# Performance work log

Hardware: AMD Instinct MI355X
Metric: run time of the kernel (lower is better)

## Reference

```python
import jax, jax.numpy as jnp
import numpy as np

B, S, N, U, E, L = 32, 32, 128, 64, 2, 2
N_STEPS = 3
NUM_CLASSES = 5


def setup_inputs() -> dict:
    key = jax.random.key(0)
    ks = jax.random.split(key, 10)
    input_seq = jax.random.normal(ks[0], (B, S, N * U), dtype=jnp.float32)
    seq_lengths = jax.random.randint(ks[1], (B,), 0, S)
    # per-edge-type adjacency, scaled ~row-stochastic for numerical sanity
    adjacency_matrix = jax.random.uniform(ks[2], (B, E, N, N), dtype=jnp.float32) / N
    sc = 1.0 / np.sqrt(U)
    W_msg = jax.random.normal(ks[3], (L, E, U, U), dtype=jnp.float32) * sc
    b_msg = jnp.zeros((L, U), dtype=jnp.float32)
    Wg = jax.random.normal(ks[4], (L, 3, U, U), dtype=jnp.float32) * sc  # gates from aggregated messages
    Ug = jax.random.normal(ks[5], (L, 3, U, U), dtype=jnp.float32) * sc  # gates from hidden state
    bg = jnp.zeros((L, 3, U), dtype=jnp.float32)
    fc_w = jax.random.normal(ks[6], (U, NUM_CLASSES), dtype=jnp.float32) * sc
    fc_b = jnp.zeros((NUM_CLASSES,), dtype=jnp.float32)
    return {
        "input_seq": input_seq, "seq_lengths": seq_lengths,
        "adjacency_matrix": adjacency_matrix,
        "W_msg": W_msg, "b_msg": b_msg, "Wg": Wg, "Ug": Ug, "bg": bg,
        "fc_w": fc_w, "fc_b": fc_b,
    }


def _ggnn_layer(h, A, W_msg_l, b_msg_l, Wg_l, Ug_l, bg_l):
    # h: [S,B,N,U], A: [B,E,N,N] (shared across timesteps)
    for _ in range(N_STEPS):
        # typed message passing: sum_e A_e @ h @ W_e
        a = jnp.einsum('benm,sbmu,euv->sbnv', A, h, W_msg_l) + b_msg_l
        g_a = jnp.einsum('sbnu,guv->gsbnv', a, Wg_l)  # [3,S,B,N,U]
        z = jax.nn.sigmoid(g_a[0] + h @ Ug_l[0] + bg_l[0])
        r = jax.nn.sigmoid(g_a[1] + h @ Ug_l[1] + bg_l[1])
        c = jnp.tanh(g_a[2] + (r * h) @ Ug_l[2] + bg_l[2])
        h = (1.0 - z) * h + z * c
    return h


def reference(input_seq, seq_lengths, adjacency_matrix, W_msg, b_msg, Wg, Ug, bg, fc_w, fc_b):
    # encoder: hidden state is NOT carried across timesteps in the original
    # (cell is called with current input only), so timesteps are vectorized.
    cur = input_seq.reshape(B, S, N, U).transpose(1, 0, 2, 3)  # [S,B,N,U]
    for l in range(L):
        cur = _ggnn_layer(cur, adjacency_matrix, W_msg[l], b_msg[l], Wg[l], Ug[l], bg[l])
    out = cur.transpose(1, 0, 2, 3)  # [B,S,N,U]
    idx = jnp.clip(seq_lengths - 1, 0, S - 1)
    last = out[jnp.arange(B), idx]  # [B,N,U] (last relevant timestep)
    # dropout is identity in eval mode
    logits = jax.nn.relu(last) @ fc_w + fc_b  # [B,N,C]
    return jnp.max(logits, axis=1)  # [B,C]
```

## Files before the change

kernel.cpp:

```cpp
#include <hip/hip_runtime.h>

#define B 32
#define S 32
#define N 128
#define U 64
#define E 2
#define NCLS 5


__device__ __forceinline__ float sigmoid_f(float x) {
    return __fdividef(1.f, 1.f + __expf(-x));
}
__device__ __forceinline__ float tanh_f(float x) {
    float t = __expf(-2.f * fabsf(x));
    float y = __fdividef(1.f - t, 1.f + t);
    return copysignf(y, x);
}
__device__ __forceinline__ float bcast(float v, int u) {
    return __uint_as_float(__builtin_amdgcn_readlane(__float_as_uint(v), u));
}

template <int FIRST, int LAST>
__global__ __launch_bounds__(256, 4) void k_step(
    const float* __restrict__ x, const int* __restrict__ lens,
    const float* __restrict__ hin, float* __restrict__ hout,
    const float* __restrict__ A, const float* __restrict__ Wmsg,
    const float* __restrict__ bmsg, const float* __restrict__ Wg,
    const float* __restrict__ Ug, const float* __restrict__ bg,
    const float* __restrict__ fcw, float* __restrict__ partial, int l) {
    __shared__ float red[4 * NCLS];
    int tid = threadIdx.x;
    int wave = tid >> 6, lane = tid & 63;
    int b = blockIdx.x >> 5;
    int j = blockIdx.x & 31;
    int row = __builtin_amdgcn_readfirstlane(j * 4 + wave);

    const float* __restrict__ hsrc;
    if (FIRST) {
        int idx = lens[b] - 1;
        idx = idx < 0 ? 0 : (idx > S - 1 ? S - 1 : idx);
        hsrc = x + (size_t)(b * S + idx) * N * U;
    } else {
        hsrc = hin + (size_t)b * N * U;
    }

    float hv = hsrc[row * U + lane];

    float s0 = 0.f, s1 = 0.f;
    {
        const float4* A0 = (const float4*)(A + (((size_t)b * E + 0) * N + row) * N);
        const float4* A1 = (const float4*)(A + (((size_t)b * E + 1) * N + row) * N);
#pragma unroll 8
        for (int m4 = 0; m4 < N / 4; ++m4) {
            float4 a0 = A0[m4], a1 = A1[m4];
            float q0 = hsrc[(m4 * 4 + 0) * U + lane];
            float q1 = hsrc[(m4 * 4 + 1) * U + lane];
            float q2 = hsrc[(m4 * 4 + 2) * U + lane];
            float q3 = hsrc[(m4 * 4 + 3) * U + lane];
            s0 = fmaf(a0.x, q0, s0); s0 = fmaf(a0.y, q1, s0);
            s0 = fmaf(a0.z, q2, s0); s0 = fmaf(a0.w, q3, s0);
            s1 = fmaf(a1.x, q0, s1); s1 = fmaf(a1.y, q1, s1);
            s1 = fmaf(a1.z, q2, s1); s1 = fmaf(a1.w, q3, s1);
        }
    }

    float av = bmsg[l * U + lane];
    {
        const float* W0 = Wmsg + (size_t)(l * E + 0) * U * U + lane;
        const float* W1 = W0 + U * U;
#pragma unroll 16
        for (int u = 0; u < U; ++u) {
            av = fmaf(bcast(s0, u), W0[u * U], av);
        }
#pragma unroll 16
        for (int u = 0; u < U; ++u) {
            av = fmaf(bcast(s1, u), W1[u * U], av);
        }
    }

    const float* Wg0 = Wg + (size_t)l * 3 * U * U + lane;
    const float* Wg1 = Wg0 + U * U;
    const float* Wg2 = Wg1 + U * U;
    const float* Ug0 = Ug + (size_t)l * 3 * U * U + lane;
    const float* Ug1 = Ug0 + U * U;
    const float* Ug2 = Ug1 + U * U;
    float accz = bg[(l * 3 + 0) * U + lane];
    float accr = bg[(l * 3 + 1) * U + lane];
    float accc = bg[(l * 3 + 2) * U + lane];
#pragma unroll 16
    for (int u = 0; u < U; ++u) {
        float w0 = Wg0[u * U], w1 = Wg1[u * U], w2 = Wg2[u * U];
        float g0 = Ug0[u * U], g1 = Ug1[u * U];
        float a = bcast(av, u);
        float h = bcast(hv, u);
        accz = fmaf(a, w0, accz); accz = fmaf(h, g0, accz);
        accr = fmaf(a, w1, accr); accr = fmaf(h, g1, accr);
        accc = fmaf(a, w2, accc);
    }
    float rg = sigmoid_f(accr);
    float rh = rg * hv;
#pragma unroll 16
    for (int u = 0; u < U; ++u) {
        accc = fmaf(bcast(rh, u), Ug2[u * U], accc);
    }
    float zg = sigmoid_f(accz);
    float hn = (1.f - zg) * hv + zg * tanh_f(accc);

    if (!LAST) {
        hout[((size_t)b * N + row) * U + lane] = hn;
    } else {
        float lg[NCLS];
        float rv = hn > 0.f ? hn : 0.f;
#pragma unroll
        for (int c = 0; c < NCLS; c++) {
            lg[c] = rv * fcw[lane * NCLS + c];
        }
#pragma unroll
        for (int off = 32; off; off >>= 1) {
#pragma unroll
            for (int c = 0; c < NCLS; c++) {
                lg[c] += __shfl_xor(lg[c], off, 64);
            }
        }
        if (lane == 0) {
#pragma unroll
            for (int c = 0; c < NCLS; c++) red[wave * NCLS + c] = lg[c];
        }
        __syncthreads();
        if (tid < NCLS) {
            float m = red[tid];
            for (int w = 1; w < 4; ++w) m = fmaxf(m, red[w * NCLS + tid]);
            partial[(size_t)(b * 32 + j) * NCLS + tid] = m;
        }
    }
}

__global__ void k_final(const float* __restrict__ partial, const float* __restrict__ fcb,
                        float* __restrict__ out) {
    int b = blockIdx.x, c = threadIdx.x;
    if (c < NCLS) {
        float m = -3.4e38f;
        for (int jj = 0; jj < 32; ++jj)
            m = fmaxf(m, partial[(size_t)(b * 32 + jj) * NCLS + c]);
        out[b * NCLS + c] = m + fcb[c];
    }
}

extern "C" void kernel_launch(void* const* d_in, const int* in_sizes, int n_in,
                              void* d_out, int out_size, void* d_ws, size_t ws_size,
                              hipStream_t stream) {
    const float* x    = (const float*)d_in[0];
    const int*   lens = (const int*)d_in[1];
    const float* A    = (const float*)d_in[2];
    const float* Wmsg = (const float*)d_in[3];
    const float* bmsg = (const float*)d_in[4];
    const float* Wg   = (const float*)d_in[5];
    const float* Ug   = (const float*)d_in[6];
    const float* bg   = (const float*)d_in[7];
    const float* fcw  = (const float*)d_in[8];
    const float* fcb  = (const float*)d_in[9];
    float* out = (float*)d_out;

    float* hA      = (float*)d_ws;
    float* hB      = hA + (size_t)B * N * U;
    float* partial = hB + (size_t)B * N * U;

    k_step<1, 0><<<B * 32, 256, 0, stream>>>(x, lens, nullptr, hA, A, Wmsg, bmsg, Wg, Ug, bg, fcw, partial, 0);
    k_step<0, 0><<<B * 32, 256, 0, stream>>>(x, lens, hA, hB, A, Wmsg, bmsg, Wg, Ug, bg, fcw, partial, 0);
    k_step<0, 0><<<B * 32, 256, 0, stream>>>(x, lens, hB, hA, A, Wmsg, bmsg, Wg, Ug, bg, fcw, partial, 0);
    k_step<0, 0><<<B * 32, 256, 0, stream>>>(x, lens, hA, hB, A, Wmsg, bmsg, Wg, Ug, bg, fcw, partial, 1);
    k_step<0, 0><<<B * 32, 256, 0, stream>>>(x, lens, hB, hA, A, Wmsg, bmsg, Wg, Ug, bg, fcw, partial, 1);
    k_step<0, 1><<<B * 32, 256, 0, stream>>>(x, lens, hA, hB, A, Wmsg, bmsg, Wg, Ug, bg, fcw, partial, 1);
    k_final<<<B, 64, 0, stream>>>(partial, fcb, out);
}
```

Before: 226.4 us.

## Fuse all GGNN steps into one persistent kernel with per-batch flag barriers

Replaces six step launches plus a final reduction with a single persistent kernel of 128 blocks (4 per batch). Each wave now handles 4 rows so weight loads are reused across rows. Blocks of the same batch synchronize between steps through an atomic counter in workspace, reset by a memset before launch. This removes launch gaps and the final kernel, but cuts the grid to 128 blocks, lowering parallelism, and relies on all four blocks of a batch being resident at once. The spin loop gives up after a fixed iteration count.

```diff
diff --git a/kernel.cpp b/kernel.cpp
--- a/kernel.cpp
+++ b/kernel.cpp
@@ -6,6 +6,8 @@
 #define U 64
 #define E 2
 #define NCLS 5
+#define NBLK 4
+#define RPW 4
 
 
 __device__ __forceinline__ float sigmoid_f(float x) {
@@ -20,129 +22,180 @@
     return __uint_as_float(__builtin_amdgcn_readlane(__float_as_uint(v), u));
 }
 
-template <int FIRST, int LAST>
-__global__ __launch_bounds__(256, 4) void k_step(
+__global__ __launch_bounds__(512) void k_all(
     const float* __restrict__ x, const int* __restrict__ lens,
-    const float* __restrict__ hin, float* __restrict__ hout,
+    float* __restrict__ hA, float* __restrict__ hB,
     const float* __restrict__ A, const float* __restrict__ Wmsg,
     const float* __restrict__ bmsg, const float* __restrict__ Wg,
     const float* __restrict__ Ug, const float* __restrict__ bg,
-    const float* __restrict__ fcw, float* __restrict__ partial, int l) {
-    __shared__ float red[4 * NCLS];
+    const float* __restrict__ fcw, const float* __restrict__ fcb,
+    float* __restrict__ partial, unsigned int* __restrict__ flags,
+    float* __restrict__ out) {
+    __shared__ float red[8 * NCLS];
     int tid = threadIdx.x;
     int wave = tid >> 6, lane = tid & 63;
-    int b = blockIdx.x >> 5;
-    int j = blockIdx.x & 31;
-    int row = __builtin_amdgcn_readfirstlane(j * 4 + wave);
-
-    const float* __restrict__ hsrc;
-    if (FIRST) {
-        int idx = lens[b] - 1;
-        idx = idx < 0 ? 0 : (idx > S - 1 ? S - 1 : idx);
-        hsrc = x + (size_t)(b * S + idx) * N * U;
-    } else {
-        hsrc = hin + (size_t)b * N * U;
-    }
-
-    float hv = hsrc[row * U + lane];
-
-    float s0 = 0.f, s1 = 0.f;
-    {
-        const float4* A0 = (const float4*)(A + (((size_t)b * E + 0) * N + row) * N);
-        const float4* A1 = (const float4*)(A + (((size_t)b * E + 1) * N + row) * N);
+    int b = blockIdx.x >> 2;
+    int q = blockIdx.x & 3;
+    int n0 = __builtin_amdgcn_readfirstlane(q * 32 + wave * RPW);
+
+    int idx = lens[b] - 1;
+    idx = idx < 0 ? 0 : (idx > S - 1 ? S - 1 : idx);
+    const float* xsrc = x + (size_t)(b * S + idx) * N * U;
+    float* h0 = hA + (size_t)b * N * U;
+    float* h1 = hB + (size_t)b * N * U;
+    unsigned int* flg = flags + b * 32;
+
+    for (int step = 0; step < 6; ++step) {
+        int l = step >= 3 ? 1 : 0;
+        const float* hsrc = (step == 0) ? xsrc : ((step & 1) ? h0 : h1);
+        float* hdst = (step & 1) ? h1 : h0;
+
+        float hv[RPW];
+#pragma unroll
+        for (int r = 0; r < RPW; ++r) hv[r] = hsrc[(n0 + r) * U + lane];
+
+        float s[RPW][E];
+#pragma unroll
+        for (int r = 0; r < RPW; ++r) { s[r][0] = 0.f; s[r][1] = 0.f; }
+        {
+            const float4* Ap[E][RPW];
+#pragma unroll
+            for (int e = 0; e < E; ++e)
+#pragma unroll
+                for (int r = 0; r < RPW; ++r)
+                    Ap[e][r] = (const float4*)(A + (((size_t)b * E + e) * N + n0 + r) * N);
+#pragma unroll 2
+            for (int m4 = 0; m4 < N / 4; ++m4) {
+                float q0 = hsrc[(m4 * 4 + 0) * U + lane];
+                float q1 = hsrc[(m4 * 4 + 1) * U + lane];
+                float q2 = hsrc[(m4 * 4 + 2) * U + lane];
+                float q3 = hsrc[(m4 * 4 + 3) * U + lane];
+#pragma unroll
+                for (int e = 0; e < E; ++e)
+#pragma unroll
+                    for (int r = 0; r < RPW; ++r) {
+                        float4 a = Ap[e][r][m4];
+                        s[r][e] = fmaf(a.x, q0, s[r][e]);
+                        s[r][e] = fmaf(a.y, q1, s[r][e]);
+                        s[r][e] = fmaf(a.z, q2, s[r][e]);
+                        s[r][e] = fmaf(a.w, q3, s[r][e]);
+                    }
+            }
+        }
+
+        float bm = bmsg[l * U + lane];
+        float av[RPW];
+#pragma unroll
+        for (int r = 0; r < RPW; ++r) av[r] = bm;
+        {
+            const float* W0 = Wmsg + (size_t)(l * E + 0) * U * U + lane;
+            const float* W1 = W0 + U * U;
+#pragma unroll 16
+            for (int u = 0; u < U; ++u) {
+                float w = W0[u * U];
+#pragma unroll
+                for (int r = 0; r < RPW; ++r) av[r] = fmaf(bcast(s[r][0], u), w, av[r]);
+            }
+#pragma unroll 16
+            for (int u = 0; u < U; ++u) {
+                float w = W1[u * U];
+#pragma unroll
+                for (int r = 0; r < RPW; ++r) av[r] = fmaf(bcast(s[r][1], u), w, av[r]);
+            }
+        }
+
+        const float* Wg0 = Wg + (size_t)l * 3 * U * U + lane;
+        const float* Wg1 = Wg0 + U * U;
+        const float* Wg2 = Wg1 + U * U;
+        const float* Ug0 = Ug + (size_t)l * 3 * U * U + lane;
+        const float* Ug1 = Ug0 + U * U;
+        const float* Ug2 = Ug1 + U * U;
+        float bz = bg[(l * 3 + 0) * U + lane];
+        float br = bg[(l * 3 + 1) * U + lane];
+        float bcc = bg[(l * 3 + 2) * U + lane];
+        float accz[RPW], accr[RPW], accc[RPW];
+#pragma unroll
+        for (int r = 0; r < RPW; ++r) { accz[r] = bz; accr[r] = br; accc[r] = bcc; }
 #pragma unroll 8
-        for (int m4 = 0; m4 < N / 4; ++m4) {
-            float4 a0 = A0[m4], a1 = A1[m4];
-            float q0 = hsrc[(m4 * 4 + 0) * U + lane];
-            float q1 = hsrc[(m4 * 4 + 1) * U + lane];
-            float q2 = hsrc[(m4 * 4 + 2) * U + lane];
-            float q3 = hsrc[(m4 * 4 + 3) * U + lane];
-            s0 = fmaf(a0.x, q0, s0); s0 = fmaf(a0.y, q1, s0);
-            s0 = fmaf(a0.z, q2, s0); s0 = fmaf(a0.w, q3, s0);
-            s1 = fmaf(a1.x, q0, s1); s1 = fmaf(a1.y, q1, s1);
-            s1 = fmaf(a1.z, q2, s1); s1 = fmaf(a1.w, q3, s1);
-        }
-    }
-
-    float av = bmsg[l * U + lane];
-    {
-        const float* W0 = Wmsg + (size_t)(l * E + 0) * U * U + lane;
-        const float* W1 = W0 + U * U;
+        for (int u = 0; u < U; ++u) {
+            float w0 = Wg0[u * U], w1 = Wg1[u * U], w2 = Wg2[u * U];
+            float g0 = Ug0[u * U], g1 = Ug1[u * U];
+#pragma unroll
+            for (int r = 0; r < RPW; ++r) {
+                float a = bcast(av[r], u);
+                float h = bcast(hv[r], u);
+                accz[r] = fmaf(a, w0, accz[r]); accz[r] = fmaf(h, g0, accz[r]);
+                accr[r] = fmaf(a, w1, accr[r]); accr[r] = fmaf(h, g1, accr[r]);
+                accc[r] = fmaf(a, w2, accc[r]);
+            }
+        }
+        float rh[RPW];
+#pragma unroll
+        for (int r = 0; r < RPW; ++r) rh[r] = sigmoid_f(accr[r]) * hv[r];
 #pragma unroll 16
         for (int u = 0; u < U; ++u) {
-            av = fmaf(bcast(s0, u), W0[u * U], av);
-        }
-#pragma unroll 16
-        for (int u = 0; u < U; ++u) {
-            av = fmaf(bcast(s1, u), W1[u * U], av);
-        }
+            float g2 = Ug2[u * U];
+#pragma unroll
+            for (int r = 0; r < RPW; ++r) accc[r] = fmaf(bcast(rh[r], u), g2, accc[r]);
+        }
+        float hn[RPW];
+#pragma unroll
+        for (int r = 0; r < RPW; ++r) {
+            float zg = sigmoid_f(accz[r]);
+            hn[r] = (1.f - zg) * hv[r] + zg * tanh_f(accc[r]);
+        }
+
+        if (step < 5) {
+#pragma unroll
+            for (int r = 0; r < RPW; ++r) hdst[(n0 + r) * U + lane] = hn[r];
+        } else {
+            float lg[RPW][NCLS];
+#pragma unroll
+            for (int r = 0; r < RPW; ++r) {
+                float rv = hn[r] > 0.f ? hn[r] : 0.f;
+#pragma unroll
+                for (int c = 0; c < NCLS; ++c) lg[r][c] = rv * fcw[lane * NCLS + c];
+            }
+#pragma unroll
+            for (int off = 32; off; off >>= 1)
+#pragma unroll
+                for (int r = 0; r < RPW; ++r)
+#pragma unroll
+                    for (int c = 0; c < NCLS; ++c) lg[r][c] += __shfl_xor(lg[r][c], off, 64);
+            if (lane == 0) {
+#pragma unroll
+                for (int c = 0; c < NCLS; ++c)
+                    red[wave * NCLS + c] =
+                        fmaxf(fmaxf(lg[0][c], lg[1][c]), fmaxf(lg[2][c], lg[3][c]));
+            }
+            __syncthreads();
+            if (tid < NCLS) {
+                float m = red[tid];
+                for (int w = 1; w < 8; ++w) m = fmaxf(m, red[w * NCLS + tid]);
+                partial[(size_t)(b * NBLK + q) * NCLS + tid] = m;
+            }
+        }
+
+        __syncthreads();
+        if (tid == 0) {
+            __threadfence();
+            atomicAdd(flg, 1u);
+            unsigned int tgt = (unsigned)NBLK * (step + 1);
+            int it = 0;
+            while (__hip_atomic_load(flg, __ATOMIC_ACQUIRE,
+                                     __HIP_MEMORY_SCOPE_AGENT) < tgt) {
+                __builtin_amdgcn_s_sleep(2);
+                if (++it > (1 << 18)) break;
+            }
+        }
+        __syncthreads();
     }
 
-    const float* Wg0 = Wg + (size_t)l * 3 * U * U + lane;
-    const float* Wg1 = Wg0 + U * U;
-    const float* Wg2 = Wg1 + U * U;
-    const float* Ug0 = Ug + (size_t)l * 3 * U * U + lane;
-    const float* Ug1 = Ug0 + U * U;
-    const float* Ug2 = Ug1 + U * U;
-    float accz = bg[(l * 3 + 0) * U + lane];
-    float accr = bg[(l * 3 + 1) * U + lane];
-    float accc = bg[(l * 3 + 2) * U + lane];
-#pragma unroll 16
-    for (int u = 0; u < U; ++u) {
-        float w0 = Wg0[u * U], w1 = Wg1[u * U], w2 = Wg2[u * U];
-        float g0 = Ug0[u * U], g1 = Ug1[u * U];
-        float a = bcast(av, u);
-        float h = bcast(hv, u);
-        accz = fmaf(a, w0, accz); accz = fmaf(h, g0, accz);
-        accr = fmaf(a, w1, accr); accr = fmaf(h, g1, accr);
-        accc = fmaf(a, w2, accc);
-    }
-    float rg = sigmoid_f(accr);
-    float rh = rg * hv;
-#pragma unroll 16
-    for (int u = 0; u < U; ++u) {
-        accc = fmaf(bcast(rh, u), Ug2[u * U], accc);
-    }
-    float zg = sigmoid_f(accz);
-    float hn = (1.f - zg) * hv + zg * tanh_f(accc);
-
-    if (!LAST) {
-        hout[((size_t)b * N + row) * U + lane] = hn;
-    } else {
-        float lg[NCLS];
-        float rv = hn > 0.f ? hn : 0.f;
-#pragma unroll
-        for (int c = 0; c < NCLS; c++) {
-            lg[c] = rv * fcw[lane * NCLS + c];
-        }
-#pragma unroll
-        for (int off = 32; off; off >>= 1) {
-#pragma unroll
-            for (int c = 0; c < NCLS; c++) {
-                lg[c] += __shfl_xor(lg[c], off, 64);
-            }
-        }
-        if (lane == 0) {
-#pragma unroll
-            for (int c = 0; c < NCLS; c++) red[wave * NCLS + c] = lg[c];
-        }
-        __syncthreads();
-        if (tid < NCLS) {
-            float m = red[tid];
-            for (int w = 1; w < 4; ++w) m = fmaxf(m, red[w * NCLS + tid]);
-            partial[(size_t)(b * 32 + j) * NCLS + tid] = m;
-        }
-    }
-}
-
-__global__ void k_final(const float* __restrict__ partial, const float* __restrict__ fcb,
-                        float* __restrict__ out) {
-    int b = blockIdx.x, c = threadIdx.x;
-    if (c < NCLS) {
+    if (q == 0 && tid < NCLS) {
         float m = -3.4e38f;
-        for (int jj = 0; jj < 32; ++jj)
-            m = fmaxf(m, partial[(size_t)(b * 32 + jj) * NCLS + c]);
-        out[b * NCLS + c] = m + fcb[c];
+        for (int jj = 0; jj < NBLK; ++jj)
+            m = fmaxf(m, partial[(size_t)(b * NBLK + jj) * NCLS + tid]);
+        out[b * NCLS + tid] = m + fcb[tid];
     }
 }
 
@@ -164,12 +217,9 @@
     float* hA      = (float*)d_ws;
     float* hB      = hA + (size_t)B * N * U;
     float* partial = hB + (size_t)B * N * U;
-
-    k_step<1, 0><<<B * 32, 256, 0, stream>>>(x, lens, nullptr, hA, A, Wmsg, bmsg, Wg, Ug, bg, fcw, partial, 0);
-    k_step<0, 0><<<B * 32, 256, 0, stream>>>(x, lens, hA, hB, A, Wmsg, bmsg, Wg, Ug, bg, fcw, partial, 0);
-    k_step<0, 0><<<B * 32, 256, 0, stream>>>(x, lens, hB, hA, A, Wmsg, bmsg, Wg, Ug, bg, fcw, partial, 0);
-    k_step<0, 0><<<B * 32, 256, 0, stream>>>(x, lens, hA, hB, A, Wmsg, bmsg, Wg, Ug, bg, fcw, partial, 1);
-    k_step<0, 0><<<B * 32, 256, 0, stream>>>(x, lens, hB, hA, A, Wmsg, bmsg, Wg, Ug, bg, fcw, partial, 1);
-    k_step<0, 1><<<B * 32, 256, 0, stream>>>(x, lens, hA, hB, A, Wmsg, bmsg, Wg, Ug, bg, fcw, partial, 1);
-    k_final<<<B, 64, 0, stream>>>(partial, fcb, out);
-}
+    unsigned int* flags = (unsigned int*)(partial + (size_t)B * NBLK * NCLS);
+
+    hipMemsetAsync(flags, 0, (size_t)B * 32 * sizeof(unsigned int), stream);
+    k_all<<<B * NBLK, 512, 0, stream>>>(x, lens, hA, hB, A, Wmsg, bmsg, Wg, Ug,
+                                        bg, fcw, fcb, partial, flags, out);
+}
```

Result: slower. 267.7 us (+18.3%).
